# Kernel optimization log

Hardware: AMD Instinct MI355X
Metric: run time of the kernel (lower is better)

The kernel has to match this reference:

```python
import math
import jax, jax.numpy as jnp
import numpy as np

V, D, DEPTH, S, B = 32000, 1024, 4, 512, 2
N, K = 16, 4            # ssm state_dim, d_conv
R = math.ceil(D / 16)   # dt_rank ('auto') = 64
MLP = 4 * D


def _ln(x, s, b):
    m = jnp.mean(x, -1, keepdims=True)
    v = jnp.mean((x - m) ** 2, -1, keepdims=True)
    return (x - m) * jax.lax.rsqrt(v + 1e-5) * s + b


def _dwconv(x, w):
    # x: [B,S,D], w: [D,1,K]; causal depthwise conv (torch pads K-1 both sides then slices [:S])
    xt = jnp.transpose(x, (0, 2, 1))  # [B,D,S]
    y = jax.lax.conv_general_dilated(
        xt, w, window_strides=(1,), padding=[(K - 1, 0)],
        feature_group_count=D, dimension_numbers=('NCH', 'OIH', 'NCH'))
    return jnp.transpose(y, (0, 2, 1))


def _ssm(x, zw, pw, cw, dw, db, al, dpar, ow):
    z = x @ zw.T                     # [B,S,D]
    p = x @ pw.T                     # [B,S,R+2N]
    dt_un, Bp, Cp = p[..., :R], p[..., R:R + N], p[..., R + N:]
    dt = jax.nn.softplus(dt_un @ dw.T + db)          # [B,S,D]
    u = jax.nn.silu(_dwconv(x, cw))                  # [B,S,D]
    A = -jnp.exp(al)                                 # [D,N]
    At = jnp.exp(dt[..., None] * A)                  # [B,S,D,N]
    Bt = jnp.where(jnp.abs(A) < 1e-8, dt[..., None], (At - 1.0) / (A + 1e-10))
    inp = jnp.einsum('bsdn,bsn,bsd->bsdn', Bt, Bp, u)

    def step(h, xs):
        At_t, inp_t, C_t = xs
        h = At_t * h + inp_t
        return h, jnp.einsum('bn,bdn->bd', C_t, h)

    h0 = jnp.zeros((x.shape[0], D, N), x.dtype)
    _, ys = jax.lax.scan(step, h0, (jnp.moveaxis(At, 1, 0), jnp.moveaxis(inp, 1, 0), jnp.moveaxis(Cp, 1, 0)))
    y = jnp.moveaxis(ys, 0, 1)                       # [B,S,D]
    y = (y + u * dpar) * jax.nn.silu(z)
    return y @ ow.T


def _forward(input_ids, timesteps, tok_emb, time_w1, time_b1, time_w2, time_b2,
             norm1_s, norm1_b, xW, zW, pW, convW, dtW, dtb, A_log, Dp, outW,
             norm2_s, norm2_b, mlpW1, mlpb1, mlpW2, mlpb2, normo_s, normo_b, headW, headb):
    half = D // 2
    inv = jnp.exp(-(math.log(10000.0) / half) * jnp.arange(half, dtype=jnp.float32))
    args = timesteps.astype(jnp.float32)[:, None] * inv
    temb = jnp.concatenate([jnp.sin(args), jnp.cos(args)], axis=-1)        # [B,D]
    temb = jax.nn.silu(temb @ time_w1.T + time_b1) @ time_w2.T + time_b2
    x = tok_emb[input_ids] + temb[:, None, :]                              # [B,S,D]

    def block(x, prm):
        n1s, n1b, zw, pw, cw, dw, db, al, dpar, ow, n2s, n2b, w1, b1, w2, b2 = prm
        x = x + _ssm(_ln(x, n1s, n1b), zw, pw, cw, dw, db, al, dpar, ow)
        xn = _ln(x, n2s, n2b)
        x = x + (jax.nn.gelu(xn @ w1.T + b1, approximate=False) @ w2.T + b2)
        return x, None

    stacked = (norm1_s, norm1_b, zW, pW, convW, dtW, dtb, A_log, Dp, outW,
               norm2_s, norm2_b, mlpW1, mlpb1, mlpW2, mlpb2)
    x, _ = jax.lax.scan(block, x, stacked)
    x = _ln(x, normo_s, normo_b)
    return x @ headW.T + headb  # [B,S,V]


def setup_inputs():
    key = jax.random.key(0)
    ks = jax.random.split(key, 24)
    rn = lambda k, sh, sc=0.02: jax.random.normal(k, sh, jnp.float32) * sc
    dt_std = R ** (-0.5) * 0.1
    inp = {
        'input_ids': jax.random.randint(ks[0], (B, S), 0, V + 1),
        'timesteps': jax.random.randint(ks[1], (B,), 0, 100),
        'tok_emb': rn(ks[2], (V + 1, D)),
        'time_w1': rn(ks[3], (4 * D, D)), 'time_b1': jnp.zeros((4 * D,), jnp.float32),
        'time_w2': rn(ks[4], (D, 4 * D)), 'time_b2': jnp.zeros((D,), jnp.float32),
        'norm1_s': jnp.ones((DEPTH, D), jnp.float32), 'norm1_b': jnp.zeros((DEPTH, D), jnp.float32),
        'xW': rn(ks[5], (DEPTH, D, D)),   # in_proj_x (dead in forward, grad=0)
        'zW': rn(ks[6], (DEPTH, D, D)),
        'pW': rn(ks[7], (DEPTH, R + 2 * N, D)),
        'convW': rn(ks[8], (DEPTH, D, 1, K), 0.1),
        'dtW': jax.random.uniform(ks[9], (DEPTH, D, R), jnp.float32, -dt_std, dt_std),
        'dtb': jnp.full((DEPTH, D), math.log(math.expm1(0.001)), jnp.float32),
        'A_log': jnp.tile(jnp.log(jnp.arange(1, N + 1, dtype=jnp.float32))[None, None, :], (DEPTH, D, 1)),
        'Dp': jnp.ones((DEPTH, D), jnp.float32),
        'outW': rn(ks[10], (DEPTH, D, D)),
        'norm2_s': jnp.ones((DEPTH, D), jnp.float32), 'norm2_b': jnp.zeros((DEPTH, D), jnp.float32),
        'mlpW1': rn(ks[11], (DEPTH, MLP, D)), 'mlpb1': jnp.zeros((DEPTH, MLP), jnp.float32),
        'mlpW2': rn(ks[12], (DEPTH, D, MLP)), 'mlpb2': jnp.zeros((DEPTH, D), jnp.float32),
        'normo_s': jnp.ones((D,), jnp.float32), 'normo_b': jnp.zeros((D,), jnp.float32),
        'headW': rn(ks[13], (V, D)), 'headb': jnp.zeros((V,), jnp.float32),
    }
    return inp


def reference(input_ids, timesteps, tok_emb, time_w1, time_b1, time_w2, time_b2,
              norm1_s, norm1_b, xW, zW, pW, convW, dtW, dtb, A_log, Dp, outW,
              norm2_s, norm2_b, mlpW1, mlpb1, mlpW2, mlpb2, normo_s, normo_b, headW, headb):
    return _forward(input_ids, timesteps, tok_emb, time_w1, time_b1, time_w2, time_b2,
                    norm1_s, norm1_b, xW, zW, pW, convW, dtW, dtb, A_log, Dp, outW,
                    norm2_s, norm2_b, mlpW1, mlpb1, mlpW2, mlpb2, normo_s, normo_b, headW, headb)
```

## Files before the change

kernel.cpp:

```cpp
#include <hip/hip_runtime.h>
#include <math.h>


#define DEV __device__ __forceinline__
typedef unsigned int u32;
typedef unsigned short ushort;
typedef __bf16 bf16x8 __attribute__((ext_vector_type(8)));
typedef float f32x4 __attribute__((ext_vector_type(4)));
typedef ushort us8 __attribute__((ext_vector_type(8)));

DEV float silu_f(float x){ return x / (1.f + expf(-x)); }
DEV float gelu_f(float x){ return 0.5f * x * (1.f + erff(x * 0.70710678118654752f)); }
DEV float softplus_f(float x){ return (x > 20.f) ? x : log1pf(expf(x)); }
DEV ushort f2b(float f){
  u32 u = __builtin_bit_cast(u32, f);
  return (ushort)((u + 0x7fffu + ((u >> 16) & 1u)) >> 16);
}
DEV float b2f(ushort u){ return __builtin_bit_cast(float, (u32)u << 16); }

DEV void gl_lds16(const ushort* g, ushort* l){
  __builtin_amdgcn_global_load_lds(
      (const __attribute__((address_space(1))) u32*)g,
      (__attribute__((address_space(3))) u32*)l, 16, 0, 0);
}

DEV us8 cvt2(float4 a, float4 b){
  us8 v;
  v[0]=f2b(a.x); v[1]=f2b(a.y); v[2]=f2b(a.z); v[3]=f2b(a.w);
  v[4]=f2b(b.x); v[5]=f2b(b.y); v[6]=f2b(b.z); v[7]=f2b(b.w);
  return v;
}

DEV void cvt_layer_unit(u32 j, const float* zWl, const float* pWl, const float* oWl,
                        const float* m1Wl, const float* m2Wl, ushort* wl)
{
  const float* src; u32 sj, dj;
  if (j < 294912u){
    dj = j;
    u32 row = j >> 8;
    if (row < 1024u){ src = zWl; sj = j; }
    else {
      u32 pr = row - 1024u;
      if (pr >= 96u){ ushort4 z4 = {0,0,0,0}; ((ushort4*)wl)[dj] = z4; return; }
      src = pWl; sj = pr*256u + (j & 255u);
    }
  } else if (j < 557056u){ u32 k = j - 294912u;  dj = j; src = oWl;  sj = k; }
  else if (j < 1605632u){ u32 k = j - 557056u;  dj = j; src = m1Wl; sj = k; }
  else                  { u32 k = j - 1605632u; dj = j; src = m2Wl; sj = k; }
  float4 v = ((const float4*)src)[sj];
  ushort4 o4; o4.x=f2b(v.x); o4.y=f2b(v.y); o4.z=f2b(v.z); o4.w=f2b(v.w);
  ((ushort4*)wl)[dj] = o4;
}

__global__ __launch_bounds__(256) void k_cvtmega(
    const float* __restrict__ zW, const float* __restrict__ pW,
    const float* __restrict__ oW, const float* __restrict__ m1W,
    const float* __restrict__ m2W, ushort* __restrict__ wall)
{
  u32 i = blockIdx.x*256u + threadIdx.x;
  if (i >= 10616832u) return;
  u32 l = i / 2654208u;
  u32 j = i - l*2654208u;
  cvt_layer_unit(j, zW + (size_t)l*1048576u, pW + (size_t)l*98304u,
                 oW + (size_t)l*1048576u, m1W + (size_t)l*4194304u,
                 m2W + (size_t)l*4194304u, wall + (size_t)l*10616832u);
}

__global__ __launch_bounds__(256) void k_cvtall(
    const float* __restrict__ zWl, const float* __restrict__ pWl,
    const float* __restrict__ oWl, const float* __restrict__ m1Wl,
    const float* __restrict__ m2Wl, ushort* __restrict__ wl)
{
  u32 j = blockIdx.x*256u + threadIdx.x;
  if (j >= 2654208u) return;
  cvt_layer_unit(j, zWl, pWl, oWl, m1Wl, m2Wl, wl);
}

__global__ __launch_bounds__(256) void k_cvt(const float* __restrict__ in, ushort* __restrict__ out, int n4){
  int i = blockIdx.x*256 + threadIdx.x;
  if (i >= n4) return;
  float4 v = ((const float4*)in)[i];
  ushort4 o; o.x=f2b(v.x); o.y=f2b(v.y); o.z=f2b(v.z); o.w=f2b(v.w);
  ((ushort4*)out)[i] = o;
}

__global__ __launch_bounds__(256) void k_temb1m(const int* __restrict__ ts, const float* __restrict__ w1,
                                                const float* __restrict__ b1, float* __restrict__ t1){
  __shared__ float sXT[1024];
  int bid = blockIdx.x;
  int tid = threadIdx.x;
  int b = (bid*4) >> 12;
  float tv = (float)ts[b];
  #pragma unroll
  for (int k=0;k<4;k++){
    int j = tid + k*256;
    int i = j & 511;
    float arg = tv * expf(-(9.210340371976184f/512.f) * (float)i);
    sXT[j] = (j < 512) ? sinf(arg) : cosf(arg);
  }
  __syncthreads();
  int o = bid*4 + (tid >> 6);
  int lane = tid & 63;
  int j = o & 4095;
  const float4* xr = (const float4*)sXT;
  const float4* wr = (const float4*)(w1 + (size_t)j*1024);
  float acc = 0.f;
  #pragma unroll
  for (int i=0;i<4;i++){
    float4 x4 = xr[i*64 + lane], w4 = wr[i*64 + lane];
    acc += x4.x*w4.x + x4.y*w4.y + x4.z*w4.z + x4.w*w4.w;
  }
  #pragma unroll
  for (int off=32; off; off>>=1) acc += __shfl_down(acc, off);
  if (lane==0) t1[o] = silu_f(acc + b1[j]);
}

__global__ __launch_bounds__(256) void k_temb2(const float* __restrict__ t1, const float* __restrict__ w2,
                                               const float* __restrict__ b2, float* __restrict__ t2){
  int o = blockIdx.x*4 + (threadIdx.x >> 6);
  int lane = threadIdx.x & 63;
  int b = o >> 10, j = o & 1023;
  const float4* xr = (const float4*)(t1 + b*4096);
  const float4* wr = (const float4*)(w2 + (size_t)j*4096);
  float acc = 0.f;
  #pragma unroll
  for (int i=0;i<16;i++){
    float4 x4 = xr[i*64 + lane], w4 = wr[i*64 + lane];
    acc += x4.x*w4.x + x4.y*w4.y + x4.z*w4.z + x4.w*w4.w;
  }
  #pragma unroll
  for (int off=32; off; off>>=1) acc += __shfl_down(acc, off);
  if (lane==0) t2[o] = acc + b2[j];
}

DEV void ln_body(float4 v, const float* sc, const float* bi, int row, int t,
                 float* o, ushort* obf)
{
  float sum = v.x+v.y+v.z+v.w;
  float sq  = v.x*v.x+v.y*v.y+v.z*v.z+v.w*v.w;
  for (int o_=32;o_;o_>>=1){ sum += __shfl_down(sum,o_); sq += __shfl_down(sq,o_); }
  __shared__ float ps[8];
  int lane = t & 63, wid = t >> 6;
  if (lane==0){ ps[wid]=sum; ps[4+wid]=sq; }
  __syncthreads();
  float tot = ps[0]+ps[1]+ps[2]+ps[3];
  float tsq = ps[4]+ps[5]+ps[6]+ps[7];
  float m = tot * (1.f/1024.f);
  float var = tsq*(1.f/1024.f) - m*m;
  float r = rsqrtf(var + 1e-5f);
  float4 s4 = ((const float4*)sc)[t];
  float4 b4 = ((const float4*)bi)[t];
  float4 o4;
  o4.x = (v.x-m)*r*s4.x + b4.x;
  o4.y = (v.y-m)*r*s4.y + b4.y;
  o4.z = (v.z-m)*r*s4.z + b4.z;
  o4.w = (v.w-m)*r*s4.w + b4.w;
  ((float4*)(o + (size_t)row*1024))[t] = o4;
  ushort4 ob; ob.x=f2b(o4.x); ob.y=f2b(o4.y); ob.z=f2b(o4.z); ob.w=f2b(o4.w);
  ((ushort4*)(obf + (size_t)row*1024))[t] = ob;
}

__global__ __launch_bounds__(256) void k_ln(const float* __restrict__ x, const float* __restrict__ sc,
                                            const float* __restrict__ bi, float* __restrict__ o,
                                            ushort* __restrict__ obf){
  int row = blockIdx.x, t = threadIdx.x;
  float4 v = ((const float4*)(x + (size_t)row*1024))[t];
  ln_body(v, sc, bi, row, t, o, obf);
}

__global__ __launch_bounds__(256) void k_embln(const int* __restrict__ ids, const float* __restrict__ tok,
                                               const float* __restrict__ t2, const float* __restrict__ sc,
                                               const float* __restrict__ bi, float* __restrict__ xout,
                                               float* __restrict__ o, ushort* __restrict__ obf){
  int row = blockIdx.x, t = threadIdx.x;
  int id = ids[row];
  float4 v = ((const float4*)(tok + (size_t)id*1024))[t];
  float4 e = ((const float4*)(t2 + ((row >> 9) << 10)))[t];
  v.x += e.x; v.y += e.y; v.z += e.z; v.w += e.w;
  ((float4*)(xout + (size_t)row*1024))[t] = v;
  ln_body(v, sc, bi, row, t, o, obf);
}

__global__ __launch_bounds__(512) void k_scanf(
    const ushort* __restrict__ pb64, const float* __restrict__ dtW, const float* __restrict__ dtb,
    const float* __restrict__ xn, const float* __restrict__ p, const float* __restrict__ alog,
    const float* __restrict__ z, const float* __restrict__ Dp,
    const float* __restrict__ cw, ushort* __restrict__ y2b)
{
  const int bid = blockIdx.x;
  const int logical = (bid & 7)*256 + (bid >> 3);
  const int d = logical & 1023;
  const int b = logical >> 10;
  const int tid = threadIdx.x;
  const int c = tid >> 4, n = tid & 15;
  const float al = alog[d*16 + n];
  const float A = -expf(al);
  const float invA = 1.f/(A + 1e-10f);
  const bool tiny = fabsf(A) < 1e-8f;
  const float dscale = Dp[d];
  const float cw0 = cw[d*4], cw1 = cw[d*4+1], cw2 = cw[d*4+2], cw3 = cw[d*4+3];
  const size_t base = (size_t)b*512*1024 + d;
  const float* pp = p + (size_t)b*512*96;
  const int s0 = c*16;

  __shared__ float sXN[520];
  __shared__ float sDT[512], sZ[512];
  __shared__ float sA[512], sB[512], sH[512];
  __shared__ float sDTW[64];

  if (tid < 64) sDTW[tid] = dtW[d*64 + tid];
  {
    int s = tid - 3;
    sXN[tid] = (s >= 0) ? xn[base + (size_t)s*1024] : 0.f;
    if (tid < 3) sXN[512 + tid] = xn[base + (size_t)(509 + tid)*1024];
    sZ[tid] = z[base + (size_t)tid*1024];
  }
  __syncthreads();

  {
    const us8* pr = (const us8*)(pb64 + (size_t)(b*512 + tid)*64);
    float acc = 0.f;
    #pragma unroll
    for (int q=0;q<8;q++){
      us8 v = pr[q];
      #pragma unroll
      for (int e=0;e<8;e++)
        acc = fmaf(b2f(v[e]), sDTW[q*8+e], acc);
    }
    sDT[tid] = softplus_f(acc + dtb[d]);
  }
  __syncthreads();

  float At[16], inp[16];
  float h = 0.f, pa = 1.f;
  #pragma unroll
  for (int s8=0; s8<16; s8++){
    int s = s0 + s8;
    float uv = silu_f(sXN[s]*cw0 + sXN[s+1]*cw1 + sXN[s+2]*cw2 + sXN[s+3]*cw3);
    float dtv = sDT[s];
    float Bpv = pp[s*96 + 64 + n];
    float a  = expf(dtv*A);
    float bt = tiny ? dtv : (a-1.f)*invA;
    At[s8] = a;
    float ip = bt*Bpv*uv;
    inp[s8] = ip;
    h = a*h + ip;
    pa *= a;
  }
  sA[tid]=pa; sB[tid]=h;
  __syncthreads();
  if (tid < 16){
    float H = 0.f;
    #pragma unroll
    for (int c2=0;c2<32;c2++){
      sH[c2*16+tid] = H;
      H = sA[c2*16+tid]*H + sB[c2*16+tid];
    }
  }
  __syncthreads();

  h = sH[tid];
  #pragma unroll
  for (int s8=0; s8<16; s8++){
    int s = s0 + s8;
    h = At[s8]*h + inp[s8];
    float Cpv = pp[s*96 + 80 + n];
    float cc = Cpv*h;
    cc += __shfl_xor(cc,1);
    cc += __shfl_xor(cc,2);
    cc += __shfl_xor(cc,4);
    cc += __shfl_xor(cc,8);
    if (n==0){
      float uv = silu_f(sXN[s]*cw0 + sXN[s+1]*cw1 + sXN[s+2]*cw2 + sXN[s+3]*cw3);
      float zv = sZ[s];
      y2b[base + (size_t)s*1024] = f2b((cc + uv*dscale) * (zv/(1.f+expf(-zv))));
    }
  }
}

template<int TM, int TN, int EPI, bool OBF>
__global__ __launch_bounds__(256) void k_bgemm(
    const ushort* __restrict__ A,
    const ushort* __restrict__ W,
    const float* __restrict__ bias,
    const float* __restrict__ resid,
    void* __restrict__ Cout,
    int ldc, int nmax, int K,
    float* __restrict__ pout, ushort* __restrict__ pbout)
{
  constexpr int WN = 2;
  constexpr int WM = 2;
  constexpr int MR = TM/(WM*16);
  constexpr int NR = TN/(WN*16);
  constexpr int LA = TM/32;
  constexpr int LB = TN/32;
  constexpr int LT = LA + LB;

  __shared__ ushort As[2][TM*64] __attribute__((aligned(16)));
  __shared__ ushort Bs[2][TN*64] __attribute__((aligned(16)));
  const int t = threadIdx.x;
  const int w = t >> 6, lane = t & 63;
  const int wn = w % WN, wm = w / WN;
  const int m0 = blockIdx.y * TM;
  const int n0 = blockIdx.x * TN;

  f32x4 acc[MR][NR];
  #pragma unroll
  for (int i=0;i<MR;i++)
    #pragma unroll
    for (int j=0;j<NR;j++) acc[i][j] = (f32x4){0.f,0.f,0.f,0.f};

  const int srow = (lane >> 3);
  const int scol = (((lane & 7) ^ srow)) * 8;

  auto issue = [&](int k0, int buf){
    #pragma unroll
    for (int i=0;i<LA;i++){
      int chunk = i*4 + w;
      int row = chunk*8 + srow;
      gl_lds16(A + (size_t)(m0 + row)*K + k0 + scol, &As[buf][chunk*512]);
    }
    #pragma unroll
    for (int i=0;i<LB;i++){
      int chunk = i*4 + w;
      int row = chunk*8 + srow;
      gl_lds16(W + (size_t)(n0 + row)*K + k0 + scol, &Bs[buf][chunk*512]);
    }
  };

  issue(0, 0);
  const int NS = K >> 6;
  const int fr = lane & 15;
  const int hi = lane >> 4;
  for (int s = 0; s < NS; ++s){
    const int cur = s & 1;
    if (s + 1 < NS){
      issue((s+1)*64, cur^1);
      asm volatile("s_waitcnt vmcnt(%0)" :: "i"(LT) : "memory");
    } else {
      asm volatile("s_waitcnt vmcnt(0)" ::: "memory");
    }
    __builtin_amdgcn_sched_barrier(0);
    __builtin_amdgcn_s_barrier();
    __builtin_amdgcn_sched_barrier(0);
    __builtin_amdgcn_s_setprio(1);
    #pragma unroll
    for (int kk=0; kk<2; ++kk){
      bf16x8 a[MR], b[NR];
      const int cofs = (((kk<<2) | hi) ^ (fr & 7)) * 8;
      #pragma unroll
      for (int am=0; am<MR; am++)
        a[am] = *(const bf16x8*)&As[cur][(wm*(MR*16) + am*16 + fr)*64 + cofs];
      #pragma unroll
      for (int bn=0; bn<NR; bn++)
        b[bn] = *(const bf16x8*)&Bs[cur][(wn*(NR*16) + bn*16 + fr)*64 + cofs];
      #pragma unroll
      for (int am=0; am<MR; am++)
        #pragma unroll
        for (int bn=0; bn<NR; bn++)
          acc[am][bn] = __builtin_amdgcn_mfma_f32_16x16x32_bf16(a[am], b[bn], acc[am][bn], 0, 0, 0);
    }
    __builtin_amdgcn_s_setprio(0);
    __builtin_amdgcn_sched_barrier(0);
    __builtin_amdgcn_s_barrier();
  }

  #pragma unroll
  for (int am=0; am<MR; am++){
    #pragma unroll
    for (int bn=0; bn<NR; bn++){
      int r0 = m0 + wm*(MR*16) + am*16 + ((lane>>4)<<2);
      int cc = n0 + wn*(NR*16) + bn*16 + (lane&15);
      if (cc >= nmax) continue;
      float bv = 0.f;
      if constexpr (EPI==1 || EPI==2 || EPI==5) bv = bias[cc];
      #pragma unroll
      for (int r=0; r<4; r++){
        float v = acc[am][bn][r];
        if constexpr (EPI==1 || EPI==2 || EPI==5) v += bv;
        if constexpr (EPI==2) v = gelu_f(v);
        if constexpr (EPI==4 || EPI==5) v += resid[(size_t)(r0+r)*ldc + cc];
        if constexpr (EPI==6){
          if (cc < 1024) ((float*)Cout)[(size_t)(r0+r)*ldc + cc] = v;
          else {
            int pc = cc - 1024;
            if (pc < 96) pout[(size_t)(r0+r)*96 + pc] = v;
            if (pc < 64) pbout[(size_t)(r0+r)*64 + pc] = f2b(v);
          }
        } else if constexpr (OBF){
          ((ushort*)Cout)[(size_t)(r0+r)*ldc + cc] = f2b(v);
        } else {
          ((float*)Cout)[(size_t)(r0+r)*ldc + cc] = v;
        }
      }
    }
  }
}

__global__ __launch_bounds__(512) void k_bgemmHF(
    const ushort* __restrict__ A,
    const float*  __restrict__ W,
    const float* __restrict__ bias,
    float* __restrict__ Cout,
    int ldc, int K)
{
  __shared__ ushort As[256*64] __attribute__((aligned(16)));
  __shared__ ushort Bs[128*64] __attribute__((aligned(16)));
  const int t = threadIdx.x;
  const int w = t >> 6, lane = t & 63;
  const int wn = w & 1, wm = w >> 1;
  const int bid = blockIdx.x;
  const int logical = (bid & 7)*125 + (bid >> 3);
  const int m0 = (logical & 3) * 256;
  const int n0 = (logical >> 2) * 128;

  f32x4 acc[4][4];
  #pragma unroll
  for (int i=0;i<4;i++)
    #pragma unroll
    for (int j=0;j<4;j++) acc[i][j] = (f32x4){0.f,0.f,0.f,0.f};

  const int srow = (lane >> 3);
  const int scolA = (((lane & 7) ^ srow)) * 8;

  const int brow = t >> 2;
  const int bq   = t & 3;
  const float* wp = W + (size_t)(n0 + brow)*K + bq*16;
  const int slot0 = ((bq*2)   ^ (brow & 7)) * 8;
  const int slot1 = ((bq*2+1) ^ (brow & 7)) * 8;

  float4 fb[4];
  #pragma unroll
  for (int j=0;j<4;j++) fb[j] = *(const float4*)(wp + j*4);

  const int fr = lane & 15;
  const int hi = lane >> 4;
  for (int k0 = 0; k0 < K; k0 += 64){
    __builtin_amdgcn_sched_barrier(0);
    __builtin_amdgcn_s_barrier();
    __builtin_amdgcn_sched_barrier(0);
    #pragma unroll
    for (int i=0;i<4;i++){
      int chunk = i*8 + w;
      int row = chunk*8 + srow;
      gl_lds16(A + (size_t)(m0 + row)*K + k0 + scolA, &As[chunk*512]);
    }
    asm volatile("s_waitcnt vmcnt(4)" ::: "memory");
    __builtin_amdgcn_sched_barrier(0);
    *(us8*)&Bs[brow*64 + slot0] = cvt2(fb[0], fb[1]);
    *(us8*)&Bs[brow*64 + slot1] = cvt2(fb[2], fb[3]);
    if (k0 + 64 < K){
      #pragma unroll
      for (int j=0;j<4;j++) fb[j] = *(const float4*)(wp + k0 + 64 + j*4);
      asm volatile("s_waitcnt vmcnt(4) lgkmcnt(0)" ::: "memory");
    } else {
      asm volatile("s_waitcnt vmcnt(0) lgkmcnt(0)" ::: "memory");
    }
    __builtin_amdgcn_sched_barrier(0);
    __builtin_amdgcn_s_barrier();
    __builtin_amdgcn_sched_barrier(0);
    __builtin_amdgcn_s_setprio(1);
    #pragma unroll
    for (int kk=0; kk<2; ++kk){
      bf16x8 a[4], b[4];
      const int cofs = (((kk<<2) | hi) ^ (fr & 7)) * 8;
      #pragma unroll
      for (int am=0; am<4; am++)
        a[am] = *(const bf16x8*)&As[(wm*64 + am*16 + fr)*64 + cofs];
      #pragma unroll
      for (int bn=0; bn<4; bn++)
        b[bn] = *(const bf16x8*)&Bs[(wn*64 + bn*16 + fr)*64 + cofs];
      #pragma unroll
      for (int am=0; am<4; am++)
        #pragma unroll
        for (int bn=0; bn<4; bn++)
          acc[am][bn] = __builtin_amdgcn_mfma_f32_16x16x32_bf16(a[am], b[bn], acc[am][bn], 0, 0, 0);
    }
    __builtin_amdgcn_s_setprio(0);
  }

  #pragma unroll
  for (int am=0; am<4; am++){
    #pragma unroll
    for (int bn=0; bn<4; bn++){
      int r0 = m0 + wm*64 + am*16 + ((lane>>4)<<2);
      int cc = n0 + wn*64 + bn*16 + (lane&15);
      float bv = bias[cc];
      #pragma unroll
      for (int r=0; r<4; r++)
        Cout[(size_t)(r0+r)*ldc + cc] = acc[am][bn][r] + bv;
    }
  }
}

extern "C" void kernel_launch(void* const* d_in, const int* in_sizes, int n_in,
                              void* d_out, int out_size, void* d_ws, size_t ws_size,
                              hipStream_t stream)
{
  const int*   ids    = (const int*)d_in[0];
  const int*   tsteps = (const int*)d_in[1];
  const float* tok    = (const float*)d_in[2];
  const float* tw1    = (const float*)d_in[3];
  const float* tb1    = (const float*)d_in[4];
  const float* tw2    = (const float*)d_in[5];
  const float* tb2    = (const float*)d_in[6];
  const float* n1s    = (const float*)d_in[7];
  const float* n1b    = (const float*)d_in[8];
  const float* zW     = (const float*)d_in[10];
  const float* pW     = (const float*)d_in[11];
  const float* cW     = (const float*)d_in[12];
  const float* dtW    = (const float*)d_in[13];
  const float* dtb    = (const float*)d_in[14];
  const float* alog   = (const float*)d_in[15];
  const float* Dp     = (const float*)d_in[16];
  const float* oW     = (const float*)d_in[17];
  const float* n2s    = (const float*)d_in[18];
  const float* n2b    = (const float*)d_in[19];
  const float* m1W    = (const float*)d_in[20];
  const float* m1b    = (const float*)d_in[21];
  const float* m2W    = (const float*)d_in[22];
  const float* m2b    = (const float*)d_in[23];
  const float* nos    = (const float*)d_in[24];
  const float* nob    = (const float*)d_in[25];
  const float* hW     = (const float*)d_in[26];
  const float* hb     = (const float*)d_in[27];

  float* ws = (float*)d_ws;
  float*  x    = ws;
  float*  xn   = ws + 1048576;
  float*  z    = ws + 2097152;
  float*  p    = ws + 3145728;
  ushort* pb64 = (ushort*)(ws + 3244032);
  float*  t1   = ws + 3276800;
  float*  t2   = ws + 3284992;
  ushort* xnb  = (ushort*)(ws + 3670016);
  ushort* y2b  = (ushort*)(ws + 4194304);
  ushort* h1b  = (ushort*)(ws + 5242880);

  const size_t WBASE = 7340032;
  const size_t WL_US = 10616832;
  const bool big = ws_size >= 179830784ull;
  ushort* wall = (ushort*)(ws + WBASE);
  ushort* whb  = (ushort*)(ws + WBASE + (big ? 4*(WL_US/2) : 0));

  dim3 blk(256);
  if (big)
    k_cvtmega<<<dim3(41472), blk, 0, stream>>>(zW, pW, oW, m1W, m2W, wall);
  k_temb1m<<<dim3(2048), blk, 0, stream>>>(tsteps, tw1, tb1, t1);
  k_temb2<<<dim3(512),  blk, 0, stream>>>(t1, tw2, tb2, t2);

  for (int l=0; l<4; l++){
    ushort* wl = wall + (big ? (size_t)l*WL_US : 0);
    ushort* wzp = wl;
    ushort* wo  = wl + 1179648;
    ushort* wm1 = wl + 2228224;
    ushort* wm2 = wl + 6422528;
    if (!big)
      k_cvtall<<<dim3(10368), blk, 0, stream>>>(
          zW + (size_t)l*1048576, pW + (size_t)l*98304, oW + (size_t)l*1048576,
          m1W + (size_t)l*4194304, m2W + (size_t)l*4194304, wl);
    if (l == 0)
      k_embln<<<dim3(1024), blk, 0, stream>>>(ids, tok, t2, n1s, n1b, x, xn, xnb);
    else
      k_ln<<<dim3(1024), blk, 0, stream>>>(x, n1s + l*1024, n1b + l*1024, xn, xnb);
    k_bgemm<64,64,6,false><<<dim3(18,16), blk, 0, stream>>>(xnb, wzp, nullptr, nullptr, z,
                                                            1024, 1152, 1024, p, pb64);
    k_scanf<<<dim3(2048), dim3(512), 0, stream>>>(pb64, dtW + (size_t)l*65536, dtb + l*1024,
                                                  xn, p, alog + l*16384, z, Dp + l*1024,
                                                  cW + l*4096, y2b);
    k_bgemm<64,64,4,false><<<dim3(16,16), blk, 0, stream>>>(y2b, wo, nullptr, x, x,
                                                            1024, 1024, 1024, nullptr, nullptr);
    k_ln<<<dim3(1024), blk, 0, stream>>>(x, n2s + l*1024, n2b + l*1024, xn, xnb);
    k_bgemm<64,64,2,true><<<dim3(64,16), blk, 0, stream>>>(xnb, wm1, m1b + l*4096, nullptr, h1b,
                                                           4096, 4096, 1024, nullptr, nullptr);
    k_bgemm<64,64,5,false><<<dim3(16,16), blk, 0, stream>>>(h1b, wm2, m2b + l*1024, x, x,
                                                            1024, 1024, 4096, nullptr, nullptr);
  }
  k_ln<<<dim3(1024), blk, 0, stream>>>(x, nos, nob, xn, xnb);

  if (big){
    k_bgemmHF<<<dim3(1000), dim3(512), 0, stream>>>(xnb, hW, hb, (float*)d_out, 32000, 1024);
  } else {
    for (int h=0; h<2; h++){
      k_cvt<<<dim3(16000), blk, 0, stream>>>(hW + (size_t)h*16384000, whb, 4096000);
      k_bgemm<128,128,1,false><<<dim3(125,8), blk, 0, stream>>>(xnb, whb, hb + h*16000, nullptr,
                                                                (float*)d_out + h*16000,
                                                                32000, 16000, 1024, nullptr, nullptr);
    }
  }
}
```

Measured before the change: 876.6 us.

## Fuse fp32-to-bf16 weight conversion into GEMM B-tile loading, drop pre-conversion passes

Removes the separate weight conversion kernels (mega-convert and per-layer convert) and instead has each GEMM load fp32 weights from global memory into registers, convert them to bf16 and store them swizzled into LDS. Register prefetching of the next weight tile replaces the double-buffered LDS async loads. The z/p projection merges its two weight sources inside the kernel. This cuts a full extra read and write of the converted weights. In exchange the GEMMs read twice the weight bytes, and every M-tile block re-converts the same weights with single-buffered LDS.

Result: slower. 947.2 us (+8.0%).

```diff
diff --git a/kernel.cpp b/kernel.cpp
--- a/kernel.cpp
+++ b/kernel.cpp
@@ -29,59 +29,6 @@
   v[0]=f2b(a.x); v[1]=f2b(a.y); v[2]=f2b(a.z); v[3]=f2b(a.w);
   v[4]=f2b(b.x); v[5]=f2b(b.y); v[6]=f2b(b.z); v[7]=f2b(b.w);
   return v;
-}
-
-DEV void cvt_layer_unit(u32 j, const float* zWl, const float* pWl, const float* oWl,
-                        const float* m1Wl, const float* m2Wl, ushort* wl)
-{
-  const float* src; u32 sj, dj;
-  if (j < 294912u){
-    dj = j;
-    u32 row = j >> 8;
-    if (row < 1024u){ src = zWl; sj = j; }
-    else {
-      u32 pr = row - 1024u;
-      if (pr >= 96u){ ushort4 z4 = {0,0,0,0}; ((ushort4*)wl)[dj] = z4; return; }
-      src = pWl; sj = pr*256u + (j & 255u);
-    }
-  } else if (j < 557056u){ u32 k = j - 294912u;  dj = j; src = oWl;  sj = k; }
-  else if (j < 1605632u){ u32 k = j - 557056u;  dj = j; src = m1Wl; sj = k; }
-  else                  { u32 k = j - 1605632u; dj = j; src = m2Wl; sj = k; }
-  float4 v = ((const float4*)src)[sj];
-  ushort4 o4; o4.x=f2b(v.x); o4.y=f2b(v.y); o4.z=f2b(v.z); o4.w=f2b(v.w);
-  ((ushort4*)wl)[dj] = o4;
-}
-
-__global__ __launch_bounds__(256) void k_cvtmega(
-    const float* __restrict__ zW, const float* __restrict__ pW,
-    const float* __restrict__ oW, const float* __restrict__ m1W,
-    const float* __restrict__ m2W, ushort* __restrict__ wall)
-{
-  u32 i = blockIdx.x*256u + threadIdx.x;
-  if (i >= 10616832u) return;
-  u32 l = i / 2654208u;
-  u32 j = i - l*2654208u;
-  cvt_layer_unit(j, zW + (size_t)l*1048576u, pW + (size_t)l*98304u,
-                 oW + (size_t)l*1048576u, m1W + (size_t)l*4194304u,
-                 m2W + (size_t)l*4194304u, wall + (size_t)l*10616832u);
-}
-
-__global__ __launch_bounds__(256) void k_cvtall(
-    const float* __restrict__ zWl, const float* __restrict__ pWl,
-    const float* __restrict__ oWl, const float* __restrict__ m1Wl,
-    const float* __restrict__ m2Wl, ushort* __restrict__ wl)
-{
-  u32 j = blockIdx.x*256u + threadIdx.x;
-  if (j >= 2654208u) return;
-  cvt_layer_unit(j, zWl, pWl, oWl, m1Wl, m2Wl, wl);
-}
-
-__global__ __launch_bounds__(256) void k_cvt(const float* __restrict__ in, ushort* __restrict__ out, int n4){
-  int i = blockIdx.x*256 + threadIdx.x;
-  if (i >= n4) return;
-  float4 v = ((const float4*)in)[i];
-  ushort4 o; o.x=f2b(v.x); o.y=f2b(v.y); o.z=f2b(v.z); o.w=f2b(v.w);
-  ((ushort4*)out)[i] = o;
 }
 
 __global__ __launch_bounds__(256) void k_temb1m(const int* __restrict__ ts, const float* __restrict__ w1,
@@ -278,67 +225,82 @@
   }
 }
 
-template<int TM, int TN, int EPI, bool OBF>
-__global__ __launch_bounds__(256) void k_bgemm(
+template<int EPI, bool OBF, bool ZP>
+__global__ __launch_bounds__(256) void k_bgemmF2(
     const ushort* __restrict__ A,
-    const ushort* __restrict__ W,
+    const float*  __restrict__ Wz,
+    const float*  __restrict__ Wp,
     const float* __restrict__ bias,
     const float* __restrict__ resid,
     void* __restrict__ Cout,
     int ldc, int nmax, int K,
     float* __restrict__ pout, ushort* __restrict__ pbout)
 {
-  constexpr int WN = 2;
-  constexpr int WM = 2;
-  constexpr int MR = TM/(WM*16);
-  constexpr int NR = TN/(WN*16);
-  constexpr int LA = TM/32;
-  constexpr int LB = TN/32;
-  constexpr int LT = LA + LB;
-
-  __shared__ ushort As[2][TM*64] __attribute__((aligned(16)));
-  __shared__ ushort Bs[2][TN*64] __attribute__((aligned(16)));
+  __shared__ ushort As[64*64] __attribute__((aligned(16)));
+  __shared__ ushort Bs[64*64] __attribute__((aligned(16)));
   const int t = threadIdx.x;
   const int w = t >> 6, lane = t & 63;
-  const int wn = w % WN, wm = w / WN;
-  const int m0 = blockIdx.y * TM;
-  const int n0 = blockIdx.x * TN;
-
-  f32x4 acc[MR][NR];
-  #pragma unroll
-  for (int i=0;i<MR;i++)
-    #pragma unroll
-    for (int j=0;j<NR;j++) acc[i][j] = (f32x4){0.f,0.f,0.f,0.f};
+  const int wn = w & 1, wm = w >> 1;
+  const int m0 = blockIdx.y * 64;
+  const int n0 = blockIdx.x * 64;
+
+  f32x4 acc[2][2];
+  #pragma unroll
+  for (int i=0;i<2;i++)
+    #pragma unroll
+    for (int j=0;j<2;j++) acc[i][j] = (f32x4){0.f,0.f,0.f,0.f};
 
   const int srow = (lane >> 3);
-  const int scol = (((lane & 7) ^ srow)) * 8;
-
-  auto issue = [&](int k0, int buf){
-    #pragma unroll
-    for (int i=0;i<LA;i++){
+  const int scolA = (((lane & 7) ^ srow)) * 8;
+
+  const int brow = t >> 2;
+  const int bq   = t & 3;
+  const int grow = n0 + brow;
+  const float* wp;
+  bool bvalid;
+  if constexpr (ZP){
+    if (grow < 1024){ wp = Wz + (size_t)grow*K + bq*16; bvalid = true; }
+    else if (grow < 1120){ wp = Wp + (size_t)(grow-1024)*K + bq*16; bvalid = true; }
+    else { wp = Wz; bvalid = false; }
+  } else {
+    wp = Wz + (size_t)grow*K + bq*16; bvalid = true;
+  }
+  const int slot0 = ((bq*2)   ^ (brow & 7)) * 8;
+  const int slot1 = ((bq*2+1) ^ (brow & 7)) * 8;
+
+  float4 fb[4] = {make_float4(0,0,0,0), make_float4(0,0,0,0),
+                  make_float4(0,0,0,0), make_float4(0,0,0,0)};
+  if (bvalid){
+    #pragma unroll
+    for (int j=0;j<4;j++) fb[j] = *(const float4*)(wp + j*4);
+  }
+
+  const int fr = lane & 15;
+  const int hi = lane >> 4;
+  for (int k0 = 0; k0 < K; k0 += 64){
+    __builtin_amdgcn_sched_barrier(0);
+    __builtin_amdgcn_s_barrier();
+    __builtin_amdgcn_sched_barrier(0);
+    #pragma unroll
+    for (int i=0;i<2;i++){
       int chunk = i*4 + w;
       int row = chunk*8 + srow;
-      gl_lds16(A + (size_t)(m0 + row)*K + k0 + scol, &As[buf][chunk*512]);
-    }
-    #pragma unroll
-    for (int i=0;i<LB;i++){
-      int chunk = i*4 + w;
-      int row = chunk*8 + srow;
-      gl_lds16(W + (size_t)(n0 + row)*K + k0 + scol, &Bs[buf][chunk*512]);
-    }
-  };
-
-  issue(0, 0);
-  const int NS = K >> 6;
-  const int fr = lane & 15;
-  const int hi = lane >> 4;
-  for (int s = 0; s < NS; ++s){
-    const int cur = s & 1;
-    if (s + 1 < NS){
-      issue((s+1)*64, cur^1);
-      asm volatile("s_waitcnt vmcnt(%0)" :: "i"(LT) : "memory");
+      gl_lds16(A + (size_t)(m0 + row)*K + k0 + scolA, &As[chunk*512]);
+    }
+    asm volatile("s_waitcnt vmcnt(2)" ::: "memory");
+    __builtin_amdgcn_sched_barrier(0);
+    *(us8*)&Bs[brow*64 + slot0] = cvt2(fb[0], fb[1]);
+    *(us8*)&Bs[brow*64 + slot1] = cvt2(fb[2], fb[3]);
+    if (k0 + 64 < K){
+      if (bvalid){
+        #pragma unroll
+        for (int j=0;j<4;j++) fb[j] = *(const float4*)(wp + k0 + 64 + j*4);
+        asm volatile("s_waitcnt vmcnt(4) lgkmcnt(0)" ::: "memory");
+      } else {
+        asm volatile("s_waitcnt vmcnt(0) lgkmcnt(0)" ::: "memory");
+      }
     } else {
-      asm volatile("s_waitcnt vmcnt(0)" ::: "memory");
+      asm volatile("s_waitcnt vmcnt(0) lgkmcnt(0)" ::: "memory");
     }
     __builtin_amdgcn_sched_barrier(0);
     __builtin_amdgcn_s_barrier();
@@ -346,38 +308,36 @@
     __builtin_amdgcn_s_setprio(1);
     #pragma unroll
     for (int kk=0; kk<2; ++kk){
-      bf16x8 a[MR], b[NR];
+      bf16x8 a[2], b[2];
       const int cofs = (((kk<<2) | hi) ^ (fr & 7)) * 8;
       #pragma unroll
-      for (int am=0; am<MR; am++)
-        a[am] = *(const bf16x8*)&As[cur][(wm*(MR*16) + am*16 + fr)*64 + cofs];
-      #pragma unroll
-      for (int bn=0; bn<NR; bn++)
-        b[bn] = *(const bf16x8*)&Bs[cur][(wn*(NR*16) + bn*16 + fr)*64 + cofs];
-      #pragma unroll
-      for (int am=0; am<MR; am++)
+      for (int am=0; am<2; am++)
+        a[am] = *(const bf16x8*)&As[(wm*32 + am*16 + fr)*64 + cofs];
+      #pragma unroll
+      for (int bn=0; bn<2; bn++)
+        b[bn] = *(const bf16x8*)&Bs[(wn*32 + bn*16 + fr)*64 + cofs];
+      #pragma unroll
+      for (int am=0; am<2; am++)
         #pragma unroll
-        for (int bn=0; bn<NR; bn++)
+        for (int bn=0; bn<2; bn++)
           acc[am][bn] = __builtin_amdgcn_mfma_f32_16x16x32_bf16(a[am], b[bn], acc[am][bn], 0, 0, 0);
     }
     __builtin_amdgcn_s_setprio(0);
-    __builtin_amdgcn_sched_barrier(0);
-    __builtin_amdgcn_s_barrier();
-  }
-
-  #pragma unroll
-  for (int am=0; am<MR; am++){
-    #pragma unroll
-    for (int bn=0; bn<NR; bn++){
-      int r0 = m0 + wm*(MR*16) + am*16 + ((lane>>4)<<2);
-      int cc = n0 + wn*(NR*16) + bn*16 + (lane&15);
+  }
+
+  #pragma unroll
+  for (int am=0; am<2; am++){
+    #pragma unroll
+    for (int bn=0; bn<2; bn++){
+      int r0 = m0 + wm*32 + am*16 + ((lane>>4)<<2);
+      int cc = n0 + wn*32 + bn*16 + (lane&15);
       if (cc >= nmax) continue;
       float bv = 0.f;
-      if constexpr (EPI==1 || EPI==2 || EPI==5) bv = bias[cc];
+      if constexpr (EPI==2 || EPI==5) bv = bias[cc];
       #pragma unroll
       for (int r=0; r<4; r++){
         float v = acc[am][bn][r];
-        if constexpr (EPI==1 || EPI==2 || EPI==5) v += bv;
+        if constexpr (EPI==2 || EPI==5) v += bv;
         if constexpr (EPI==2) v = gelu_f(v);
         if constexpr (EPI==4 || EPI==5) v += resid[(size_t)(r0+r)*ldc + cc];
         if constexpr (EPI==6){
@@ -537,55 +497,33 @@
   ushort* y2b  = (ushort*)(ws + 4194304);
   ushort* h1b  = (ushort*)(ws + 5242880);
 
-  const size_t WBASE = 7340032;
-  const size_t WL_US = 10616832;
-  const bool big = ws_size >= 179830784ull;
-  ushort* wall = (ushort*)(ws + WBASE);
-  ushort* whb  = (ushort*)(ws + WBASE + (big ? 4*(WL_US/2) : 0));
-
   dim3 blk(256);
-  if (big)
-    k_cvtmega<<<dim3(41472), blk, 0, stream>>>(zW, pW, oW, m1W, m2W, wall);
   k_temb1m<<<dim3(2048), blk, 0, stream>>>(tsteps, tw1, tb1, t1);
   k_temb2<<<dim3(512),  blk, 0, stream>>>(t1, tw2, tb2, t2);
 
   for (int l=0; l<4; l++){
-    ushort* wl = wall + (big ? (size_t)l*WL_US : 0);
-    ushort* wzp = wl;
-    ushort* wo  = wl + 1179648;
-    ushort* wm1 = wl + 2228224;
-    ushort* wm2 = wl + 6422528;
-    if (!big)
-      k_cvtall<<<dim3(10368), blk, 0, stream>>>(
-          zW + (size_t)l*1048576, pW + (size_t)l*98304, oW + (size_t)l*1048576,
-          m1W + (size_t)l*4194304, m2W + (size_t)l*4194304, wl);
     if (l == 0)
       k_embln<<<dim3(1024), blk, 0, stream>>>(ids, tok, t2, n1s, n1b, x, xn, xnb);
     else
       k_ln<<<dim3(1024), blk, 0, stream>>>(x, n1s + l*1024, n1b + l*1024, xn, xnb);
-    k_bgemm<64,64,6,false><<<dim3(18,16), blk, 0, stream>>>(xnb, wzp, nullptr, nullptr, z,
-                                                            1024, 1152, 1024, p, pb64);
+    k_bgemmF2<6,false,true><<<dim3(18,16), blk, 0, stream>>>(
+        xnb, zW + (size_t)l*1048576, pW + (size_t)l*98304, nullptr, nullptr,
+        z, 1024, 1152, 1024, p, pb64);
     k_scanf<<<dim3(2048), dim3(512), 0, stream>>>(pb64, dtW + (size_t)l*65536, dtb + l*1024,
                                                   xn, p, alog + l*16384, z, Dp + l*1024,
                                                   cW + l*4096, y2b);
-    k_bgemm<64,64,4,false><<<dim3(16,16), blk, 0, stream>>>(y2b, wo, nullptr, x, x,
-                                                            1024, 1024, 1024, nullptr, nullptr);
+    k_bgemmF2<4,false,false><<<dim3(16,16), blk, 0, stream>>>(
+        y2b, oW + (size_t)l*1048576, nullptr, nullptr, x,
+        x, 1024, 1024, 1024, nullptr, nullptr);
     k_ln<<<dim3(1024), blk, 0, stream>>>(x, n2s + l*1024, n2b + l*1024, xn, xnb);
-    k_bgemm<64,64,2,true><<<dim3(64,16), blk, 0, stream>>>(xnb, wm1, m1b + l*4096, nullptr, h1b,
-                                                           4096, 4096, 1024, nullptr, nullptr);
-    k_bgemm<64,64,5,false><<<dim3(16,16), blk, 0, stream>>>(h1b, wm2, m2b + l*1024, x, x,
-                                                            1024, 1024, 4096, nullptr, nullptr);
+    k_bgemmF2<2,true,false><<<dim3(64,16), blk, 0, stream>>>(
+        xnb, m1W + (size_t)l*4194304, nullptr, m1b + l*4096, nullptr,
+        h1b, 4096, 4096, 1024, nullptr, nullptr);
+    k_bgemmF2<5,false,false><<<dim3(16,16), blk, 0, stream>>>(
+        h1b, m2W + (size_t)l*4194304, nullptr, m2b + l*1024, x,
+        x, 1024, 1024, 4096, nullptr, nullptr);
   }
   k_ln<<<dim3(1024), blk, 0, stream>>>(x, nos, nob, xn, xnb);
 
-  if (big){
-    k_bgemmHF<<<dim3(1000), dim3(512), 0, stream>>>(xnb, hW, hb, (float*)d_out, 32000, 1024);
-  } else {
-    for (int h=0; h<2; h++){
-      k_cvt<<<dim3(16000), blk, 0, stream>>>(hW + (size_t)h*16384000, whb, 4096000);
-      k_bgemm<128,128,1,false><<<dim3(125,8), blk, 0, stream>>>(xnb, whb, hb + h*16000, nullptr,
-                                                                (float*)d_out + h*16000,
-                                                                32000, 16000, 1024, nullptr, nullptr);
-    }
-  }
-}
+  k_bgemmHF<<<dim3(1000), dim3(512), 0, stream>>>(xnb, hW, hb, (float*)d_out, 32000, 1024);
+}
```
